# Kernel tuning notes

Hardware: AMD Instinct MI355X
Metric: run time of the kernel (lower is better)

The kernel has to match this reference:

```python
import jax, jax.numpy as jnp
import numpy as np

N_NODES = 100000
N_EDGES = 625000
HIDDEN = 128
N_LAYERS = 4
NUM_GRAPHS = 512
INPUT_DIM = 28
EDGE_DIM = 4
OUT_DIM = 1


def setup_inputs() -> dict:
    key = jax.random.key(0)
    ks = jax.random.split(key, 16)
    x = jax.random.randint(ks[0], (N_NODES, 1), 0, INPUT_DIM)
    edge_index = jax.random.randint(ks[1], (2, N_EDGES), 0, N_NODES)
    edge_attr = jax.random.randint(ks[2], (N_EDGES,), 0, EDGE_DIM)
    batch = jnp.sort(jax.random.randint(ks[3], (N_NODES,), 0, NUM_GRAPHS))
    s = 1.0 / np.sqrt(HIDDEN)
    node_emb = jax.random.normal(ks[4], (INPUT_DIM, HIDDEN), jnp.float32)
    edge_emb = jax.random.normal(ks[5], (EDGE_DIM, HIDDEN), jnp.float32)
    conv_W1 = jax.random.normal(ks[6], (N_LAYERS, HIDDEN, HIDDEN), jnp.float32) * s
    conv_b1 = jnp.zeros((N_LAYERS, HIDDEN), jnp.float32)
    conv_W2 = jax.random.normal(ks[7], (N_LAYERS, HIDDEN, HIDDEN), jnp.float32) * s
    conv_b2 = jnp.zeros((N_LAYERS, HIDDEN), jnp.float32)
    mlp_W1 = jax.random.normal(ks[8], (HIDDEN, HIDDEN // 2), jnp.float32) * s
    mlp_b1 = jnp.zeros((HIDDEN // 2,), jnp.float32)
    mlp_W2 = jax.random.normal(ks[9], (HIDDEN // 2, HIDDEN // 4), jnp.float32) * (1.0 / np.sqrt(HIDDEN // 2))
    mlp_b2 = jnp.zeros((HIDDEN // 4,), jnp.float32)
    mlp_W3 = jax.random.normal(ks[10], (HIDDEN // 4, OUT_DIM), jnp.float32) * (1.0 / np.sqrt(HIDDEN // 4))
    mlp_b3 = jnp.zeros((OUT_DIM,), jnp.float32)
    return dict(x=x, edge_index=edge_index, edge_attr=edge_attr, batch=batch,
                node_emb=node_emb, edge_emb=edge_emb,
                conv_W1=conv_W1, conv_b1=conv_b1, conv_W2=conv_W2, conv_b2=conv_b2,
                mlp_W1=mlp_W1, mlp_b1=mlp_b1, mlp_W2=mlp_W2, mlp_b2=mlp_b2,
                mlp_W3=mlp_W3, mlp_b3=mlp_b3)


def reference(x, edge_index, edge_attr, batch, node_emb, edge_emb,
              conv_W1, conv_b1, conv_W2, conv_b2,
              mlp_W1, mlp_b1, mlp_W2, mlp_b2, mlp_W3, mlp_b3):
    h = node_emb[x[:, 0]]                    # [N, H] embedding lookup (x.squeeze(-1))
    _attr = edge_emb[edge_attr]              # computed in original forward but unused by GINConv
    src, dst = edge_index[0], edge_index[1]
    for l in range(N_LAYERS):
        # GINConv (eps=0): mlp((1+eps)*x + sum_{j->i} x_j)
        agg = jax.ops.segment_sum(h[src], dst, num_segments=N_NODES)  # [N, H]
        z = agg + h
        z = jax.nn.relu(z @ conv_W1[l] + conv_b1[l])
        h = z @ conv_W2[l] + conv_b2[l]
    g = jax.ops.segment_sum(h, batch, num_segments=NUM_GRAPHS)        # global_add_pool [G, H]
    g = jax.nn.relu(g @ mlp_W1 + mlp_b1)
    g = jax.nn.relu(g @ mlp_W2 + mlp_b2)
    return g @ mlp_W3 + mlp_b3               # [G, 1]
```

## Files before the change

### kernel.cpp

```cpp
#include <hip/hip_runtime.h>

#define N_NODES 100000
#define N_EDGES 625000
#define HIDDEN 128
#define NUM_GRAPHS 512
#define CAP 40
#define PADN 100096

typedef unsigned int uint;
typedef unsigned short ushort;
typedef short v8s __attribute__((ext_vector_type(8)));
typedef float v16f __attribute__((ext_vector_type(16)));

__device__ __forceinline__ float b2f_lo(uint u) { return __uint_as_float(u << 16); }
__device__ __forceinline__ float b2f_hi(uint u) { return __uint_as_float(u & 0xffff0000u); }
__device__ __forceinline__ uint f2b(float f) {
  uint u = __float_as_uint(f);
  return (u + 0x7fffu + ((u >> 16) & 1u)) >> 16;
}

__global__ __launch_bounds__(256) void wtrans_k(const float* __restrict__ W1,
                                                const float* __restrict__ W2,
                                                ushort* __restrict__ Wt) {
  int mat = blockIdx.x;
  const float* W = ((mat & 1) ? W2 : W1) + (size_t)(mat >> 1) * 16384;
  ushort* o = Wt + (size_t)mat * 16384;
#pragma unroll
  for (int j = 0; j < 64; j++) {
    int idx = threadIdx.x + 256 * j;
    int k = idx >> 7, n = idx & 127;
    int c = n >> 5, l31 = n & 31;
    int ks = k >> 4, khalf = (k >> 3) & 1, e = k & 7;
    o[(((c * 8 + ks) << 6) + (khalf << 5) + l31) * 8 + e] = (ushort)f2b(W[idx]);
  }
}

__global__ __launch_bounds__(256) void embed_k(const int* __restrict__ x,
                                               const float* __restrict__ emb,
                                               ushort* __restrict__ h) {
  int t = blockIdx.x * 256 + threadIdx.x;
  int n = t >> 4;
  if (n >= N_NODES) return;
  int c = t & 15;
  const float4* e = (const float4*)(emb + (size_t)x[n] * HIDDEN + c * 8);
  float4 a = e[0], b = e[1];
  uint4 o;
  o.x = f2b(a.x) | (f2b(a.y) << 16);
  o.y = f2b(a.z) | (f2b(a.w) << 16);
  o.z = f2b(b.x) | (f2b(b.y) << 16);
  o.w = f2b(b.z) | (f2b(b.w) << 16);
  ((uint4*)h)[t] = o;
}

__global__ __launch_bounds__(256) void build_k(const int* __restrict__ src,
                                               const int* __restrict__ dst,
                                               int* __restrict__ cursor,
                                               int* __restrict__ slots) {
  int e = blockIdx.x * 256 + threadIdx.x;
  if (e >= N_EDGES) return;
  int d = dst[e];
  int p = atomicAdd(&cursor[d], 1);
  if (p < CAP) slots[(size_t)d * CAP + p] = src[e];
}

__global__ __launch_bounds__(256) void hist_k(const int* __restrict__ cursor,
                                              int* __restrict__ bins) {
  __shared__ int lb[CAP + 1];
  int tid = threadIdx.x;
  if (tid <= CAP) lb[tid] = 0;
  __syncthreads();
  int n = blockIdx.x * 256 + tid;
  if (n < N_NODES) {
    int d = cursor[n]; if (d > CAP) d = CAP;
    atomicAdd(&lb[d], 1);
  }
  __syncthreads();
  if (tid <= CAP && lb[tid] > 0) atomicAdd(&bins[tid], lb[tid]);
}

__global__ __launch_bounds__(64) void scan_k(int* __restrict__ bins) {
  int i = threadIdx.x;
  int c = (i <= CAP) ? bins[i] : 0;
  int incl = c;
#pragma unroll
  for (int off = 1; off < 64; off <<= 1) {
    int t = __shfl_up(incl, off, 64);
    if (i >= off) incl += t;
  }
  if (i <= CAP) bins[i] = incl - c;
}

__global__ __launch_bounds__(256) void scatter_k(const int* __restrict__ cursor,
                                                 int* __restrict__ bins,
                                                 int* __restrict__ perm) {
  __shared__ int lb[CAP + 1];
  __shared__ int lbase[CAP + 1];
  int tid = threadIdx.x;
  if (tid <= CAP) lb[tid] = 0;
  __syncthreads();
  int n = blockIdx.x * 256 + tid;
  int d = 0, rank = 0;
  bool real = (n < N_NODES);
  if (real) {
    d = cursor[n]; if (d > CAP) d = CAP;
    rank = atomicAdd(&lb[d], 1);
  }
  __syncthreads();
  if (tid <= CAP) {
    int c = lb[tid];
    lbase[tid] = c > 0 ? atomicAdd(&bins[tid], c) : 0;
  }
  __syncthreads();
  if (real) perm[(N_NODES - 1) - (lbase[d] + rank)] = n;
  else if (n < PADN) perm[n] = 0;
}

__device__ __forceinline__ void loadrow(uint4 dst[8], const uint4* __restrict__ rowp,
                                        int khalf) {
#pragma unroll
  for (int ks = 0; ks < 8; ks++) dst[ks] = rowp[khalf + 2 * ks];
}

__device__ __forceinline__ void accum8(const uint4 u[8], float acc[8][8]) {
#pragma unroll
  for (int ks = 0; ks < 8; ks++) {
    acc[ks][0] += b2f_lo(u[ks].x); acc[ks][1] += b2f_hi(u[ks].x);
    acc[ks][2] += b2f_lo(u[ks].y); acc[ks][3] += b2f_hi(u[ks].y);
    acc[ks][4] += b2f_lo(u[ks].z); acc[ks][5] += b2f_hi(u[ks].z);
    acc[ks][6] += b2f_lo(u[ks].w); acc[ks][7] += b2f_hi(u[ks].w);
  }
}

__global__ __launch_bounds__(64, 3) void layer_k(const ushort* __restrict__ hin,
                                                 const int* __restrict__ cursor,
                                                 const int* __restrict__ slots,
                                                 const int* __restrict__ perm,
                                                 const ushort* __restrict__ W1f,
                                                 const ushort* __restrict__ W2f,
                                                 const float* __restrict__ b1,
                                                 const float* __restrict__ b2,
                                                 ushort* __restrict__ hout) {
  int lane = threadIdx.x;
  int l31 = lane & 31;
  int khalf = lane >> 5;
  int tb = blockIdx.x * 32;
  int prow = perm[tb + l31];
  bool valid = (tb + l31) < N_NODES;

  float acc[8][8];
#pragma unroll
  for (int ks = 0; ks < 8; ks++)
#pragma unroll
    for (int e = 0; e < 8; e++) acc[ks][e] = 0.f;

  const uint4* base = (const uint4*)hin;
  uint4 A[8], B[8];
  loadrow(A, base + (size_t)prow * 16, khalf);

  int deg = valid ? cursor[prow] : 0;
  if (deg > CAP) deg = CAP;
  const int* sl = slots + (size_t)prow * CAP;
  if (deg > 0) loadrow(B, base + (size_t)sl[0] * 16, khalf);
  __builtin_amdgcn_sched_barrier(0);
  accum8(A, acc);

  int j = 0;
  while (j + 2 <= deg) {
    loadrow(A, base + (size_t)sl[j + 1] * 16, khalf);
    __builtin_amdgcn_sched_barrier(0);
    accum8(B, acc);
    if (j + 2 < deg) loadrow(B, base + (size_t)sl[j + 2] * 16, khalf);
    __builtin_amdgcn_sched_barrier(0);
    accum8(A, acc);
    j += 2;
  }
  if (j < deg) accum8(B, acc);

  union U { uint4 u; v8s s; };
  U afr[8];
#pragma unroll
  for (int ks = 0; ks < 8; ks++) {
    afr[ks].u.x = f2b(acc[ks][0]) | (f2b(acc[ks][1]) << 16);
    afr[ks].u.y = f2b(acc[ks][2]) | (f2b(acc[ks][3]) << 16);
    afr[ks].u.z = f2b(acc[ks][4]) | (f2b(acc[ks][5]) << 16);
    afr[ks].u.w = f2b(acc[ks][6]) | (f2b(acc[ks][7]) << 16);
  }

  const uint4* W1v = (const uint4*)W1f;
  v16f acc1[4] = {};
#pragma unroll
  for (int c = 0; c < 4; c++)
#pragma unroll
    for (int ks = 0; ks < 8; ks++) {
      U b; b.u = W1v[((c * 8 + ks) << 6) + lane];
      acc1[c] = __builtin_amdgcn_mfma_f32_32x32x16_bf16(b.s, afr[ks].s, acc1[c], 0, 0, 0);
    }

  uint u[4][4][2];
#pragma unroll
  for (int c = 0; c < 4; c++)
#pragma unroll
    for (int b = 0; b < 4; b++)
#pragma unroll
      for (int ap = 0; ap < 2; ap++) {
        int r0 = 2 * ap + 4 * b, r1 = r0 + 1;
        float v0 = fmaxf(acc1[c][r0] + b1[c * 32 + 2 * ap + 8 * b + 4 * khalf], 0.f);
        float v1 = fmaxf(acc1[c][r1] + b1[c * 32 + 2 * ap + 1 + 8 * b + 4 * khalf], 0.f);
        u[c][b][ap] = f2b(v0) | (f2b(v1) << 16);
      }

  uint got[4][2][2];
#pragma unroll
  for (int c = 0; c < 4; c++)
#pragma unroll
    for (int bh = 0; bh < 2; bh++)
#pragma unroll
      for (int ap = 0; ap < 2; ap++) {
        uint send = khalf ? u[c][2 * bh][ap] : u[c][2 * bh + 1][ap];
        got[c][bh][ap] = __shfl_xor(send, 32, 64);
      }

  U az[8];
#pragma unroll
  for (int ks = 0; ks < 8; ks++) {
    uint o0 = khalf ? u[ks >> 1][2 * (ks & 1) + 1][0] : u[ks >> 1][2 * (ks & 1)][0];
    uint o1 = khalf ? u[ks >> 1][2 * (ks & 1) + 1][1] : u[ks >> 1][2 * (ks & 1)][1];
    uint g0 = got[ks >> 1][ks & 1][0];
    uint g1 = got[ks >> 1][ks & 1][1];
    az[ks].u.x = khalf ? g0 : o0;
    az[ks].u.y = khalf ? g1 : o1;
    az[ks].u.z = khalf ? o0 : g0;
    az[ks].u.w = khalf ? o1 : g1;
  }

  const uint4* W2v = (const uint4*)W2f;
  v16f acc2[4] = {};
#pragma unroll
  for (int c = 0; c < 4; c++)
#pragma unroll
    for (int ks = 0; ks < 8; ks++) {
      U b; b.u = W2v[((c * 8 + ks) << 6) + lane];
      acc2[c] = __builtin_amdgcn_mfma_f32_32x32x16_bf16(az[ks].s, b.s, acc2[c], 0, 0, 0);
    }

  int trow[16];
#pragma unroll
  for (int r = 0; r < 16; r++) {
    int m = (r & 3) + 8 * (r >> 2) + 4 * khalf;
    trow[r] = __shfl(prow, m, 64);
  }
  float bv2[4];
#pragma unroll
  for (int c = 0; c < 4; c++) bv2[c] = b2[c * 32 + l31];
#pragma unroll
  for (int c = 0; c < 4; c++) {
    int col = c * 32 + l31;
#pragma unroll
    for (int r = 0; r < 16; r++) {
      int m = (r & 3) + 8 * (r >> 2) + 4 * khalf;
      if (tb + m < N_NODES)
        hout[(size_t)trow[r] * HIDDEN + col] = (ushort)f2b(acc2[c][r] + bv2[c]);
    }
  }
}

__global__ __launch_bounds__(256) void poolmlp_k(const ushort* __restrict__ h,
                                                 const int* __restrict__ batch,
                                                 const float* __restrict__ W1, const float* __restrict__ b1,
                                                 const float* __restrict__ W2, const float* __restrict__ b2,
                                                 const float* __restrict__ W3, const float* __restrict__ b3,
                                                 float* __restrict__ out) {
  __shared__ int se[2];
  __shared__ float red[16][16][8];
  __shared__ float gl[128];
  __shared__ float r2[64];
  __shared__ float r3[32];
  int gi = blockIdx.x, tid = threadIdx.x;
  if (tid < 2) {
    int target = gi + tid;
    int lo = 0, hi = N_NODES;
    while (lo < hi) {
      int mid = (lo + hi) >> 1;
      if (batch[mid] < target) lo = mid + 1; else hi = mid;
    }
    se[tid] = lo;
  }
  __syncthreads();
  int start = se[0], end = se[1];
  int cg = tid & 15, rg = tid >> 4;
  float acc[8] = {0.f, 0.f, 0.f, 0.f, 0.f, 0.f, 0.f, 0.f};
  for (int r = start + rg; r < end; r += 16) {
    uint4 v = ((const uint4*)h)[r * 16 + cg];
    acc[0] += b2f_lo(v.x); acc[1] += b2f_hi(v.x);
    acc[2] += b2f_lo(v.y); acc[3] += b2f_hi(v.y);
    acc[4] += b2f_lo(v.z); acc[5] += b2f_hi(v.z);
    acc[6] += b2f_lo(v.w); acc[7] += b2f_hi(v.w);
  }
#pragma unroll
  for (int j = 0; j < 8; j++) red[rg][cg][j] = acc[j];
  __syncthreads();
  if (rg == 0) {
    float s[8];
#pragma unroll
    for (int j = 0; j < 8; j++) s[j] = red[0][cg][j];
#pragma unroll
    for (int i = 1; i < 16; i++)
#pragma unroll
      for (int j = 0; j < 8; j++) s[j] += red[i][cg][j];
#pragma unroll
    for (int j = 0; j < 8; j++) gl[cg * 8 + j] = s[j];
  }
  __syncthreads();
  if (tid < 64) {
    float s = b1[tid];
    for (int k = 0; k < 128; k++) s = fmaf(gl[k], W1[k * 64 + tid], s);
    r2[tid] = fmaxf(s, 0.f);
  }
  __syncthreads();
  if (tid < 32) {
    float s2 = b2[tid];
    for (int k = 0; k < 64; k++) s2 = fmaf(r2[k], W2[k * 32 + tid], s2);
    r3[tid] = fmaxf(s2, 0.f);
  }
  __syncthreads();
  if (tid < 64) {
    float pv = (tid < 32) ? r3[tid] * W3[tid] : 0.f;
#pragma unroll
    for (int off = 32; off > 0; off >>= 1) pv += __shfl_down(pv, off);
    if (tid == 0) out[gi] = pv + b3[0];
  }
}

extern "C" void kernel_launch(void* const* d_in, const int* in_sizes, int n_in,
                              void* d_out, int out_size, void* d_ws, size_t ws_size,
                              hipStream_t stream) {
  const int* x = (const int*)d_in[0];
  const int* src = (const int*)d_in[1];
  const int* dst = src + N_EDGES;
  const int* batch = (const int*)d_in[3];
  const float* node_emb = (const float*)d_in[4];
  const float* cW1 = (const float*)d_in[6];
  const float* cb1 = (const float*)d_in[7];
  const float* cW2 = (const float*)d_in[8];
  const float* cb2 = (const float*)d_in[9];
  const float* mW1 = (const float*)d_in[10];
  const float* mb1 = (const float*)d_in[11];
  const float* mW2 = (const float*)d_in[12];
  const float* mb2 = (const float*)d_in[13];
  const float* mW3 = (const float*)d_in[14];
  const float* mb3 = (const float*)d_in[15];
  float* out = (float*)d_out;

  char* p = (char*)d_ws;
  const size_t HB = (size_t)N_NODES * HIDDEN * sizeof(ushort);
  ushort* h = (ushort*)p;      p += HB;
  ushort* t0 = (ushort*)p;     p += HB;
  ushort* Wtb = (ushort*)p;    p += (size_t)8 * 16384 * sizeof(ushort);
  int* cursor = (int*)p;       p += (size_t)N_NODES * sizeof(int);
  int* bins = (int*)p;         p += 64 * sizeof(int);
  int* slots = (int*)p;        p += (size_t)N_NODES * CAP * sizeof(int);
  int* perm = (int*)p;         p += (size_t)PADN * sizeof(int);

  hipMemsetAsync(cursor, 0, ((size_t)N_NODES + 64) * sizeof(int), stream);
  wtrans_k<<<8, 256, 0, stream>>>(cW1, cW2, Wtb);
  embed_k<<<(N_NODES * 16 + 255) / 256, 256, 0, stream>>>(x, node_emb, h);
  build_k<<<(N_EDGES + 255) / 256, 256, 0, stream>>>(src, dst, cursor, slots);
  hist_k<<<PADN / 256, 256, 0, stream>>>(cursor, bins);
  scan_k<<<1, 64, 0, stream>>>(bins);
  scatter_k<<<PADN / 256, 256, 0, stream>>>(cursor, bins, perm);

  const int grid = PADN / 32;
  ushort* bufs[2] = {h, t0};
  for (int l = 0; l < 4; l++) {
    layer_k<<<grid, 64, 0, stream>>>(bufs[l & 1], cursor, slots, perm,
                                     Wtb + (size_t)(2 * l) * 16384,
                                     Wtb + (size_t)(2 * l + 1) * 16384,
                                     cb1 + (size_t)l * HIDDEN,
                                     cb2 + (size_t)l * HIDDEN,
                                     bufs[(l & 1) ^ 1]);
  }
  poolmlp_k<<<NUM_GRAPHS, 256, 0, stream>>>(h, batch, mW1, mb1, mW2, mb2, mW3, mb3, out);
}
```

Measured before the change: 355.7 us.

## Fuse embedding lookup into first layer and triple-buffer neighbor gathers

Removes the separate embedding kernel: the first GIN layer gathers fp32 embedding rows directly via x indices and rounds them to bf16 on the fly, so the bf16 node feature buffer is never written or re-read. The main layer kernel now keeps three neighbor rows in flight instead of two and prefetches slot indices one step ahead, lowering the launch-bounds occupancy hint from 3 to 2 waves to make room for the extra registers. The shared MLP tail is factored into a helper. The trade-off is more register pressure and lower occupancy in exchange for deeper memory-level parallelism. The fused first layer also reads 2x wider fp32 rows, though the embedding table is tiny and cache-resident.

```diff
diff --git a/kernel.cpp b/kernel.cpp
--- a/kernel.cpp
+++ b/kernel.cpp
@@ -18,6 +18,9 @@
   uint u = __float_as_uint(f);
   return (u + 0x7fffu + ((u >> 16) & 1u)) >> 16;
 }
+__device__ __forceinline__ float rbf(float f) {
+  return __uint_as_float(f2b(f) << 16);
+}
 
 __global__ __launch_bounds__(256) void wtrans_k(const float* __restrict__ W1,
                                                 const float* __restrict__ W2,
@@ -33,23 +36,6 @@
     int ks = k >> 4, khalf = (k >> 3) & 1, e = k & 7;
     o[(((c * 8 + ks) << 6) + (khalf << 5) + l31) * 8 + e] = (ushort)f2b(W[idx]);
   }
-}
-
-__global__ __launch_bounds__(256) void embed_k(const int* __restrict__ x,
-                                               const float* __restrict__ emb,
-                                               ushort* __restrict__ h) {
-  int t = blockIdx.x * 256 + threadIdx.x;
-  int n = t >> 4;
-  if (n >= N_NODES) return;
-  int c = t & 15;
-  const float4* e = (const float4*)(emb + (size_t)x[n] * HIDDEN + c * 8);
-  float4 a = e[0], b = e[1];
-  uint4 o;
-  o.x = f2b(a.x) | (f2b(a.y) << 16);
-  o.y = f2b(a.z) | (f2b(a.w) << 16);
-  o.z = f2b(b.x) | (f2b(b.y) << 16);
-  o.w = f2b(b.z) | (f2b(b.w) << 16);
-  ((uint4*)h)[t] = o;
 }
 
 __global__ __launch_bounds__(256) void build_k(const int* __restrict__ src,
@@ -115,6 +101,94 @@
   else if (n < PADN) perm[n] = 0;
 }
 
+union U { uint4 u; v8s s; };
+
+__device__ __forceinline__ void gemm_tail(const U afr[8],
+                                          const ushort* __restrict__ W1f,
+                                          const ushort* __restrict__ W2f,
+                                          const float* __restrict__ b1,
+                                          const float* __restrict__ b2,
+                                          ushort* __restrict__ hout,
+                                          int lane, int l31, int khalf,
+                                          int tb, int prow) {
+  const uint4* W1v = (const uint4*)W1f;
+  v16f acc1[4] = {};
+#pragma unroll
+  for (int c = 0; c < 4; c++)
+#pragma unroll
+    for (int ks = 0; ks < 8; ks++) {
+      U b; b.u = W1v[((c * 8 + ks) << 6) + lane];
+      acc1[c] = __builtin_amdgcn_mfma_f32_32x32x16_bf16(b.s, afr[ks].s, acc1[c], 0, 0, 0);
+    }
+
+  uint u[4][4][2];
+#pragma unroll
+  for (int c = 0; c < 4; c++)
+#pragma unroll
+    for (int b = 0; b < 4; b++)
+#pragma unroll
+      for (int ap = 0; ap < 2; ap++) {
+        int r0 = 2 * ap + 4 * b, r1 = r0 + 1;
+        float v0 = fmaxf(acc1[c][r0] + b1[c * 32 + 2 * ap + 8 * b + 4 * khalf], 0.f);
+        float v1 = fmaxf(acc1[c][r1] + b1[c * 32 + 2 * ap + 1 + 8 * b + 4 * khalf], 0.f);
+        u[c][b][ap] = f2b(v0) | (f2b(v1) << 16);
+      }
+
+  uint got[4][2][2];
+#pragma unroll
+  for (int c = 0; c < 4; c++)
+#pragma unroll
+    for (int bh = 0; bh < 2; bh++)
+#pragma unroll
+      for (int ap = 0; ap < 2; ap++) {
+        uint send = khalf ? u[c][2 * bh][ap] : u[c][2 * bh + 1][ap];
+        got[c][bh][ap] = __shfl_xor(send, 32, 64);
+      }
+
+  U az[8];
+#pragma unroll
+  for (int ks = 0; ks < 8; ks++) {
+    uint o0 = khalf ? u[ks >> 1][2 * (ks & 1) + 1][0] : u[ks >> 1][2 * (ks & 1)][0];
+    uint o1 = khalf ? u[ks >> 1][2 * (ks & 1) + 1][1] : u[ks >> 1][2 * (ks & 1)][1];
+    uint g0 = got[ks >> 1][ks & 1][0];
+    uint g1 = got[ks >> 1][ks & 1][1];
+    az[ks].u.x = khalf ? g0 : o0;
+    az[ks].u.y = khalf ? g1 : o1;
+    az[ks].u.z = khalf ? o0 : g0;
+    az[ks].u.w = khalf ? o1 : g1;
+  }
+
+  const uint4* W2v = (const uint4*)W2f;
+  v16f acc2[4] = {};
+#pragma unroll
+  for (int c = 0; c < 4; c++)
+#pragma unroll
+    for (int ks = 0; ks < 8; ks++) {
+      U b; b.u = W2v[((c * 8 + ks) << 6) + lane];
+      acc2[c] = __builtin_amdgcn_mfma_f32_32x32x16_bf16(az[ks].s, b.s, acc2[c], 0, 0, 0);
+    }
+
+  int trow[16];
+#pragma unroll
+  for (int r = 0; r < 16; r++) {
+    int m = (r & 3) + 8 * (r >> 2) + 4 * khalf;
+    trow[r] = __shfl(prow, m, 64);
+  }
+  float bv2[4];
+#pragma unroll
+  for (int c = 0; c < 4; c++) bv2[c] = b2[c * 32 + l31];
+#pragma unroll
+  for (int c = 0; c < 4; c++) {
+    int col = c * 32 + l31;
+#pragma unroll
+    for (int r = 0; r < 16; r++) {
+      int m = (r & 3) + 8 * (r >> 2) + 4 * khalf;
+      if (tb + m < N_NODES)
+        hout[(size_t)trow[r] * HIDDEN + col] = (ushort)f2b(acc2[c][r] + bv2[c]);
+    }
+  }
+}
+
 __device__ __forceinline__ void loadrow(uint4 dst[8], const uint4* __restrict__ rowp,
                                         int khalf) {
 #pragma unroll
@@ -131,7 +205,7 @@
   }
 }
 
-__global__ __launch_bounds__(64, 3) void layer_k(const ushort* __restrict__ hin,
+__global__ __launch_bounds__(64, 2) void layer_k(const ushort* __restrict__ hin,
                                                  const int* __restrict__ cursor,
                                                  const int* __restrict__ slots,
                                                  const int* __restrict__ perm,
@@ -154,29 +228,37 @@
     for (int e = 0; e < 8; e++) acc[ks][e] = 0.f;
 
   const uint4* base = (const uint4*)hin;
-  uint4 A[8], B[8];
+  uint4 A[8], B[8], C[8];
   loadrow(A, base + (size_t)prow * 16, khalf);
 
   int deg = valid ? cursor[prow] : 0;
   if (deg > CAP) deg = CAP;
   const int* sl = slots + (size_t)prow * CAP;
   if (deg > 0) loadrow(B, base + (size_t)sl[0] * 16, khalf);
+  if (deg > 1) loadrow(C, base + (size_t)sl[1] * 16, khalf);
+  int sA = (deg > 2) ? sl[2] : 0;
   __builtin_amdgcn_sched_barrier(0);
   accum8(A, acc);
 
   int j = 0;
-  while (j + 2 <= deg) {
-    loadrow(A, base + (size_t)sl[j + 1] * 16, khalf);
+  while (j + 3 <= deg) {
+    loadrow(A, base + (size_t)sA * 16, khalf);
+    int sB = (j + 3 < deg) ? sl[j + 3] : 0;
     __builtin_amdgcn_sched_barrier(0);
     accum8(B, acc);
-    if (j + 2 < deg) loadrow(B, base + (size_t)sl[j + 2] * 16, khalf);
+    loadrow(B, base + (size_t)sB * 16, khalf);
+    int sC = (j + 4 < deg) ? sl[j + 4] : 0;
+    __builtin_amdgcn_sched_barrier(0);
+    accum8(C, acc);
+    loadrow(C, base + (size_t)sC * 16, khalf);
+    sA = (j + 5 < deg) ? sl[j + 5] : 0;
     __builtin_amdgcn_sched_barrier(0);
     accum8(A, acc);
-    j += 2;
+    j += 3;
   }
   if (j < deg) accum8(B, acc);
-
-  union U { uint4 u; v8s s; };
+  if (j + 1 < deg) accum8(C, acc);
+
   U afr[8];
 #pragma unroll
   for (int ks = 0; ks < 8; ks++) {
@@ -186,82 +268,84 @@
     afr[ks].u.w = f2b(acc[ks][6]) | (f2b(acc[ks][7]) << 16);
   }
 
-  const uint4* W1v = (const uint4*)W1f;
-  v16f acc1[4] = {};
-#pragma unroll
-  for (int c = 0; c < 4; c++)
-#pragma unroll
-    for (int ks = 0; ks < 8; ks++) {
-      U b; b.u = W1v[((c * 8 + ks) << 6) + lane];
-      acc1[c] = __builtin_amdgcn_mfma_f32_32x32x16_bf16(b.s, afr[ks].s, acc1[c], 0, 0, 0);
-    }
-
-  uint u[4][4][2];
-#pragma unroll
-  for (int c = 0; c < 4; c++)
-#pragma unroll
-    for (int b = 0; b < 4; b++)
-#pragma unroll
-      for (int ap = 0; ap < 2; ap++) {
-        int r0 = 2 * ap + 4 * b, r1 = r0 + 1;
-        float v0 = fmaxf(acc1[c][r0] + b1[c * 32 + 2 * ap + 8 * b + 4 * khalf], 0.f);
-        float v1 = fmaxf(acc1[c][r1] + b1[c * 32 + 2 * ap + 1 + 8 * b + 4 * khalf], 0.f);
-        u[c][b][ap] = f2b(v0) | (f2b(v1) << 16);
-      }
-
-  uint got[4][2][2];
-#pragma unroll
-  for (int c = 0; c < 4; c++)
-#pragma unroll
-    for (int bh = 0; bh < 2; bh++)
-#pragma unroll
-      for (int ap = 0; ap < 2; ap++) {
-        uint send = khalf ? u[c][2 * bh][ap] : u[c][2 * bh + 1][ap];
-        got[c][bh][ap] = __shfl_xor(send, 32, 64);
-      }
-
-  U az[8];
-#pragma unroll
-  for (int ks = 0; ks < 8; ks++) {
-    uint o0 = khalf ? u[ks >> 1][2 * (ks & 1) + 1][0] : u[ks >> 1][2 * (ks & 1)][0];
-    uint o1 = khalf ? u[ks >> 1][2 * (ks & 1) + 1][1] : u[ks >> 1][2 * (ks & 1)][1];
-    uint g0 = got[ks >> 1][ks & 1][0];
-    uint g1 = got[ks >> 1][ks & 1][1];
-    az[ks].u.x = khalf ? g0 : o0;
-    az[ks].u.y = khalf ? g1 : o1;
-    az[ks].u.z = khalf ? o0 : g0;
-    az[ks].u.w = khalf ? o1 : g1;
-  }
-
-  const uint4* W2v = (const uint4*)W2f;
-  v16f acc2[4] = {};
-#pragma unroll
-  for (int c = 0; c < 4; c++)
-#pragma unroll
-    for (int ks = 0; ks < 8; ks++) {
-      U b; b.u = W2v[((c * 8 + ks) << 6) + lane];
-      acc2[c] = __builtin_amdgcn_mfma_f32_32x32x16_bf16(az[ks].s, b.s, acc2[c], 0, 0, 0);
-    }
-
-  int trow[16];
-#pragma unroll
-  for (int r = 0; r < 16; r++) {
-    int m = (r & 3) + 8 * (r >> 2) + 4 * khalf;
-    trow[r] = __shfl(prow, m, 64);
-  }
-  float bv2[4];
-#pragma unroll
-  for (int c = 0; c < 4; c++) bv2[c] = b2[c * 32 + l31];
-#pragma unroll
-  for (int c = 0; c < 4; c++) {
-    int col = c * 32 + l31;
-#pragma unroll
-    for (int r = 0; r < 16; r++) {
-      int m = (r & 3) + 8 * (r >> 2) + 4 * khalf;
-      if (tb + m < N_NODES)
-        hout[(size_t)trow[r] * HIDDEN + col] = (ushort)f2b(acc2[c][r] + bv2[c]);
-    }
-  }
+  gemm_tail(afr, W1f, W2f, b1, b2, hout, lane, l31, khalf, tb, prow);
+}
+
+__device__ __forceinline__ void loadrow_emb(float4 dst[16], const float* __restrict__ row,
+                                            int khalf) {
+  const float4* rp = (const float4*)row;
+#pragma unroll
+  for (int ks = 0; ks < 8; ks++) {
+    dst[2 * ks]     = rp[4 * ks + 2 * khalf];
+    dst[2 * ks + 1] = rp[4 * ks + 2 * khalf + 1];
+  }
+}
+
+__device__ __forceinline__ void accum_emb(const float4 u[16], float acc[8][8]) {
+#pragma unroll
+  for (int ks = 0; ks < 8; ks++) {
+    acc[ks][0] += rbf(u[2 * ks].x);     acc[ks][1] += rbf(u[2 * ks].y);
+    acc[ks][2] += rbf(u[2 * ks].z);     acc[ks][3] += rbf(u[2 * ks].w);
+    acc[ks][4] += rbf(u[2 * ks + 1].x); acc[ks][5] += rbf(u[2 * ks + 1].y);
+    acc[ks][6] += rbf(u[2 * ks + 1].z); acc[ks][7] += rbf(u[2 * ks + 1].w);
+  }
+}
+
+__global__ __launch_bounds__(64, 2) void layer1_k(const int* __restrict__ x,
+                                                  const float* __restrict__ emb,
+                                                  const int* __restrict__ cursor,
+                                                  const int* __restrict__ slots,
+                                                  const int* __restrict__ perm,
+                                                  const ushort* __restrict__ W1f,
+                                                  const ushort* __restrict__ W2f,
+                                                  const float* __restrict__ b1,
+                                                  const float* __restrict__ b2,
+                                                  ushort* __restrict__ hout) {
+  int lane = threadIdx.x;
+  int l31 = lane & 31;
+  int khalf = lane >> 5;
+  int tb = blockIdx.x * 32;
+  int prow = perm[tb + l31];
+  bool valid = (tb + l31) < N_NODES;
+
+  float acc[8][8];
+#pragma unroll
+  for (int ks = 0; ks < 8; ks++)
+#pragma unroll
+    for (int e = 0; e < 8; e++) acc[ks][e] = 0.f;
+
+  float4 A[16], B[16];
+  loadrow_emb(A, emb + (size_t)x[prow] * HIDDEN, khalf);
+
+  int deg = valid ? cursor[prow] : 0;
+  if (deg > CAP) deg = CAP;
+  const int* sl = slots + (size_t)prow * CAP;
+  if (deg > 0) loadrow_emb(B, emb + (size_t)x[sl[0]] * HIDDEN, khalf);
+  __builtin_amdgcn_sched_barrier(0);
+  accum_emb(A, acc);
+
+  int j = 0;
+  while (j + 2 <= deg) {
+    loadrow_emb(A, emb + (size_t)x[sl[j + 1]] * HIDDEN, khalf);
+    __builtin_amdgcn_sched_barrier(0);
+    accum_emb(B, acc);
+    if (j + 2 < deg) loadrow_emb(B, emb + (size_t)x[sl[j + 2]] * HIDDEN, khalf);
+    __builtin_amdgcn_sched_barrier(0);
+    accum_emb(A, acc);
+    j += 2;
+  }
+  if (j < deg) accum_emb(B, acc);
+
+  U afr[8];
+#pragma unroll
+  for (int ks = 0; ks < 8; ks++) {
+    afr[ks].u.x = f2b(acc[ks][0]) | (f2b(acc[ks][1]) << 16);
+    afr[ks].u.y = f2b(acc[ks][2]) | (f2b(acc[ks][3]) << 16);
+    afr[ks].u.z = f2b(acc[ks][4]) | (f2b(acc[ks][5]) << 16);
+    afr[ks].u.w = f2b(acc[ks][6]) | (f2b(acc[ks][7]) << 16);
+  }
+
+  gemm_tail(afr, W1f, W2f, b1, b2, hout, lane, l31, khalf, tb, prow);
 }
 
 __global__ __launch_bounds__(256) void poolmlp_k(const ushort* __restrict__ h,
@@ -361,23 +445,25 @@
   int* slots = (int*)p;        p += (size_t)N_NODES * CAP * sizeof(int);
   int* perm = (int*)p;         p += (size_t)PADN * sizeof(int);
 
-  hipMemsetAsync(cursor, 0, ((size_t)N_NODES + 64) * sizeof(int), stream);
+  (void)hipMemsetAsync(cursor, 0, ((size_t)N_NODES + 64) * sizeof(int), stream);
   wtrans_k<<<8, 256, 0, stream>>>(cW1, cW2, Wtb);
-  embed_k<<<(N_NODES * 16 + 255) / 256, 256, 0, stream>>>(x, node_emb, h);
   build_k<<<(N_EDGES + 255) / 256, 256, 0, stream>>>(src, dst, cursor, slots);
   hist_k<<<PADN / 256, 256, 0, stream>>>(cursor, bins);
   scan_k<<<1, 64, 0, stream>>>(bins);
   scatter_k<<<PADN / 256, 256, 0, stream>>>(cursor, bins, perm);
 
   const int grid = PADN / 32;
-  ushort* bufs[2] = {h, t0};
-  for (int l = 0; l < 4; l++) {
-    layer_k<<<grid, 64, 0, stream>>>(bufs[l & 1], cursor, slots, perm,
-                                     Wtb + (size_t)(2 * l) * 16384,
-                                     Wtb + (size_t)(2 * l + 1) * 16384,
-                                     cb1 + (size_t)l * HIDDEN,
-                                     cb2 + (size_t)l * HIDDEN,
-                                     bufs[(l & 1) ^ 1]);
-  }
+  layer1_k<<<grid, 64, 0, stream>>>(x, node_emb, cursor, slots, perm,
+                                    Wtb, Wtb + 16384, cb1, cb2, t0);
+  layer_k<<<grid, 64, 0, stream>>>(t0, cursor, slots, perm,
+                                   Wtb + 2 * 16384, Wtb + 3 * 16384,
+                                   cb1 + HIDDEN, cb2 + HIDDEN, h);
+  layer_k<<<grid, 64, 0, stream>>>(h, cursor, slots, perm,
+                                   Wtb + 4 * 16384, Wtb + 5 * 16384,
+                                   cb1 + 2 * HIDDEN, cb2 + 2 * HIDDEN, t0);
+  layer_k<<<grid, 64, 0, stream>>>(t0, cursor, slots, perm,
+                                   Wtb + 6 * 16384, Wtb + 7 * 16384,
+                                   cb1 + 3 * HIDDEN, cb2 + 3 * HIDDEN, h);
+
   poolmlp_k<<<NUM_GRAPHS, 256, 0, stream>>>(h, batch, mW1, mb1, mW2, mb2, mW3, mb3, out);
 }
```

Result: slower. 383.6 us (+7.9%).

## Split neighbor gather across two waves with LDS reduction before MFMA tail

Applied to the files above, without the earlier changes.

Each layer block now runs two wavefronts for 32 nodes. Wave 0 gathers the self row plus the even neighbors, wave 1 gathers the odd neighbors. Wave 1 writes its partial sums to shared memory, and after a barrier wave 0 adds them in and runs the unchanged MFMA GEMM tail. The aim is to double the memory-level parallelism of the latency-bound gather. In exchange it adds a 16KB LDS round trip and a sync, and wave 1 sits idle during the GEMM.

```diff
diff --git a/kernel.cpp b/kernel.cpp
--- a/kernel.cpp
+++ b/kernel.cpp
@@ -115,77 +115,16 @@
   else if (n < PADN) perm[n] = 0;
 }
 
-__device__ __forceinline__ void loadrow(uint4 dst[8], const uint4* __restrict__ rowp,
-                                        int khalf) {
-#pragma unroll
-  for (int ks = 0; ks < 8; ks++) dst[ks] = rowp[khalf + 2 * ks];
-}
-
-__device__ __forceinline__ void accum8(const uint4 u[8], float acc[8][8]) {
-#pragma unroll
-  for (int ks = 0; ks < 8; ks++) {
-    acc[ks][0] += b2f_lo(u[ks].x); acc[ks][1] += b2f_hi(u[ks].x);
-    acc[ks][2] += b2f_lo(u[ks].y); acc[ks][3] += b2f_hi(u[ks].y);
-    acc[ks][4] += b2f_lo(u[ks].z); acc[ks][5] += b2f_hi(u[ks].z);
-    acc[ks][6] += b2f_lo(u[ks].w); acc[ks][7] += b2f_hi(u[ks].w);
-  }
-}
-
-__global__ __launch_bounds__(64, 3) void layer_k(const ushort* __restrict__ hin,
-                                                 const int* __restrict__ cursor,
-                                                 const int* __restrict__ slots,
-                                                 const int* __restrict__ perm,
-                                                 const ushort* __restrict__ W1f,
-                                                 const ushort* __restrict__ W2f,
-                                                 const float* __restrict__ b1,
-                                                 const float* __restrict__ b2,
-                                                 ushort* __restrict__ hout) {
-  int lane = threadIdx.x;
-  int l31 = lane & 31;
-  int khalf = lane >> 5;
-  int tb = blockIdx.x * 32;
-  int prow = perm[tb + l31];
-  bool valid = (tb + l31) < N_NODES;
-
-  float acc[8][8];
-#pragma unroll
-  for (int ks = 0; ks < 8; ks++)
-#pragma unroll
-    for (int e = 0; e < 8; e++) acc[ks][e] = 0.f;
-
-  const uint4* base = (const uint4*)hin;
-  uint4 A[8], B[8];
-  loadrow(A, base + (size_t)prow * 16, khalf);
-
-  int deg = valid ? cursor[prow] : 0;
-  if (deg > CAP) deg = CAP;
-  const int* sl = slots + (size_t)prow * CAP;
-  if (deg > 0) loadrow(B, base + (size_t)sl[0] * 16, khalf);
-  __builtin_amdgcn_sched_barrier(0);
-  accum8(A, acc);
-
-  int j = 0;
-  while (j + 2 <= deg) {
-    loadrow(A, base + (size_t)sl[j + 1] * 16, khalf);
-    __builtin_amdgcn_sched_barrier(0);
-    accum8(B, acc);
-    if (j + 2 < deg) loadrow(B, base + (size_t)sl[j + 2] * 16, khalf);
-    __builtin_amdgcn_sched_barrier(0);
-    accum8(A, acc);
-    j += 2;
-  }
-  if (j < deg) accum8(B, acc);
-
-  union U { uint4 u; v8s s; };
-  U afr[8];
-#pragma unroll
-  for (int ks = 0; ks < 8; ks++) {
-    afr[ks].u.x = f2b(acc[ks][0]) | (f2b(acc[ks][1]) << 16);
-    afr[ks].u.y = f2b(acc[ks][2]) | (f2b(acc[ks][3]) << 16);
-    afr[ks].u.z = f2b(acc[ks][4]) | (f2b(acc[ks][5]) << 16);
-    afr[ks].u.w = f2b(acc[ks][6]) | (f2b(acc[ks][7]) << 16);
-  }
-
+union U { uint4 u; v8s s; };
+
+__device__ __forceinline__ void gemm_tail(const U afr[8],
+                                          const ushort* __restrict__ W1f,
+                                          const ushort* __restrict__ W2f,
+                                          const float* __restrict__ b1,
+                                          const float* __restrict__ b2,
+                                          ushort* __restrict__ hout,
+                                          int lane, int l31, int khalf,
+                                          int tb, int prow) {
   const uint4* W1v = (const uint4*)W1f;
   v16f acc1[4] = {};
 #pragma unroll
@@ -262,6 +201,103 @@
         hout[(size_t)trow[r] * HIDDEN + col] = (ushort)f2b(acc2[c][r] + bv2[c]);
     }
   }
+}
+
+__device__ __forceinline__ void loadrow(uint4 dst[8], const uint4* __restrict__ rowp,
+                                        int khalf) {
+#pragma unroll
+  for (int ks = 0; ks < 8; ks++) dst[ks] = rowp[khalf + 2 * ks];
+}
+
+__device__ __forceinline__ void accum8(const uint4 u[8], float acc[8][8]) {
+#pragma unroll
+  for (int ks = 0; ks < 8; ks++) {
+    acc[ks][0] += b2f_lo(u[ks].x); acc[ks][1] += b2f_hi(u[ks].x);
+    acc[ks][2] += b2f_lo(u[ks].y); acc[ks][3] += b2f_hi(u[ks].y);
+    acc[ks][4] += b2f_lo(u[ks].z); acc[ks][5] += b2f_hi(u[ks].z);
+    acc[ks][6] += b2f_lo(u[ks].w); acc[ks][7] += b2f_hi(u[ks].w);
+  }
+}
+
+__global__ __launch_bounds__(128, 3) void layer_k(const ushort* __restrict__ hin,
+                                                  const int* __restrict__ cursor,
+                                                  const int* __restrict__ slots,
+                                                  const int* __restrict__ perm,
+                                                  const ushort* __restrict__ W1f,
+                                                  const ushort* __restrict__ W2f,
+                                                  const float* __restrict__ b1,
+                                                  const float* __restrict__ b2,
+                                                  ushort* __restrict__ hout) {
+  __shared__ float4 red[1024];
+  int tid = threadIdx.x;
+  int lane = tid & 63;
+  int wv = tid >> 6;
+  int l31 = lane & 31;
+  int khalf = lane >> 5;
+  int tb = blockIdx.x * 32;
+  int prow = perm[tb + l31];
+  bool valid = (tb + l31) < N_NODES;
+
+  float acc[8][8];
+#pragma unroll
+  for (int ks = 0; ks < 8; ks++)
+#pragma unroll
+    for (int e = 0; e < 8; e++) acc[ks][e] = 0.f;
+
+  const uint4* base = (const uint4*)hin;
+  int deg = valid ? cursor[prow] : 0;
+  if (deg > CAP) deg = CAP;
+  const int* sl = slots + (size_t)prow * CAP;
+
+  int m = wv ? (deg >> 1) : 1 + ((deg + 1) >> 1);
+  uint4 A[8], B[8];
+  if (m > 0) loadrow(A, base + (size_t)(wv ? sl[1] : prow) * 16, khalf);
+  if (m > 1) loadrow(B, base + (size_t)(wv ? sl[3] : sl[0]) * 16, khalf);
+  __builtin_amdgcn_sched_barrier(0);
+  if (m > 0) accum8(A, acc);
+  int i = 1;
+  while (i + 1 < m) {
+    int rA = wv ? sl[2 * (i + 1) + 1] : sl[2 * (i + 1) - 2];
+    loadrow(A, base + (size_t)rA * 16, khalf);
+    __builtin_amdgcn_sched_barrier(0);
+    accum8(B, acc);
+    if (i + 2 < m) {
+      int rB = wv ? sl[2 * (i + 2) + 1] : sl[2 * (i + 2) - 2];
+      loadrow(B, base + (size_t)rB * 16, khalf);
+    }
+    __builtin_amdgcn_sched_barrier(0);
+    accum8(A, acc);
+    i += 2;
+  }
+  if (i < m) accum8(B, acc);
+
+  if (wv == 1) {
+#pragma unroll
+    for (int ks = 0; ks < 8; ks++) {
+      red[(ks * 2 + 0) * 64 + lane] = make_float4(acc[ks][0], acc[ks][1], acc[ks][2], acc[ks][3]);
+      red[(ks * 2 + 1) * 64 + lane] = make_float4(acc[ks][4], acc[ks][5], acc[ks][6], acc[ks][7]);
+    }
+  }
+  __syncthreads();
+  if (wv == 1) return;
+#pragma unroll
+  for (int ks = 0; ks < 8; ks++) {
+    float4 v0 = red[(ks * 2 + 0) * 64 + lane];
+    float4 v1 = red[(ks * 2 + 1) * 64 + lane];
+    acc[ks][0] += v0.x; acc[ks][1] += v0.y; acc[ks][2] += v0.z; acc[ks][3] += v0.w;
+    acc[ks][4] += v1.x; acc[ks][5] += v1.y; acc[ks][6] += v1.z; acc[ks][7] += v1.w;
+  }
+
+  U afr[8];
+#pragma unroll
+  for (int ks = 0; ks < 8; ks++) {
+    afr[ks].u.x = f2b(acc[ks][0]) | (f2b(acc[ks][1]) << 16);
+    afr[ks].u.y = f2b(acc[ks][2]) | (f2b(acc[ks][3]) << 16);
+    afr[ks].u.z = f2b(acc[ks][4]) | (f2b(acc[ks][5]) << 16);
+    afr[ks].u.w = f2b(acc[ks][6]) | (f2b(acc[ks][7]) << 16);
+  }
+
+  gemm_tail(afr, W1f, W2f, b1, b2, hout, lane, l31, khalf, tb, prow);
 }
 
 __global__ __launch_bounds__(256) void poolmlp_k(const ushort* __restrict__ h,
@@ -361,7 +397,7 @@
   int* slots = (int*)p;        p += (size_t)N_NODES * CAP * sizeof(int);
   int* perm = (int*)p;         p += (size_t)PADN * sizeof(int);
 
-  hipMemsetAsync(cursor, 0, ((size_t)N_NODES + 64) * sizeof(int), stream);
+  (void)hipMemsetAsync(cursor, 0, ((size_t)N_NODES + 64) * sizeof(int), stream);
   wtrans_k<<<8, 256, 0, stream>>>(cW1, cW2, Wtb);
   embed_k<<<(N_NODES * 16 + 255) / 256, 256, 0, stream>>>(x, node_emb, h);
   build_k<<<(N_EDGES + 255) / 256, 256, 0, stream>>>(src, dst, cursor, slots);
@@ -372,12 +408,12 @@
   const int grid = PADN / 32;
   ushort* bufs[2] = {h, t0};
   for (int l = 0; l < 4; l++) {
-    layer_k<<<grid, 64, 0, stream>>>(bufs[l & 1], cursor, slots, perm,
-                                     Wtb + (size_t)(2 * l) * 16384,
-                                     Wtb + (size_t)(2 * l + 1) * 16384,
-                                     cb1 + (size_t)l * HIDDEN,
-                                     cb2 + (size_t)l * HIDDEN,
-                                     bufs[(l & 1) ^ 1]);
+    layer_k<<<grid, 128, 0, stream>>>(bufs[l & 1], cursor, slots, perm,
+                                      Wtb + (size_t)(2 * l) * 16384,
+                                      Wtb + (size_t)(2 * l + 1) * 16384,
+                                      cb1 + (size_t)l * HIDDEN,
+                                      cb2 + (size_t)l * HIDDEN,
+                                      bufs[(l & 1) ^ 1]);
   }
   poolmlp_k<<<NUM_GRAPHS, 256, 0, stream>>>(h, batch, mW1, mb1, mW2, mb2, mW3, mb3, out);
 }
```

New measurement: 361.1 us. About the same (+1.5%).
